# Optimization experiments

Hardware: AMD Instinct MI355X
Metric: run time of the kernel (lower is better)

The kernel has to match this reference:

```python
import jax, jax.numpy as jnp
import numpy as np

B, N, TS, TT, C, H, L = 64, 128, 48, 12, 3, 128, 2


def _u(key, shape, fan):
    s = 1.0 / np.sqrt(fan)
    return jax.random.uniform(key, shape, jnp.float32, -s, s)


def setup_inputs() -> dict:
    key = jax.random.key(0)
    ks = jax.random.split(key, 24)
    return {
        'flow_x': jax.random.normal(ks[0], (B, N, TS, C), jnp.float32),
        'flow_y': jax.random.normal(ks[1], (B, N, TT, C), jnp.float32),
        'enc_w_ih0': _u(ks[2], (3 * H, C), H),
        'enc_w_ih1': _u(ks[3], (3 * H, H), H),
        'enc_w_hh': _u(ks[4], (L, 3 * H, H), H),
        'enc_b_ih': _u(ks[5], (L, 3 * H), H),
        'enc_b_hh': _u(ks[6], (L, 3 * H), H),
        'enc_hid_w': _u(ks[7], (H, H), H),
        'enc_hid_b': _u(ks[8], (H,), H),
        'dec_w_ih0': _u(ks[9], (3 * H, C + H), H),
        'dec_w_ih1': _u(ks[10], (3 * H, H), H),
        'dec_w_hh': _u(ks[11], (L, 3 * H, H), H),
        'dec_b_ih': _u(ks[12], (L, 3 * H), H),
        'dec_b_hh': _u(ks[13], (L, 3 * H), H),
        'attn_w': _u(ks[14], (H, 2 * H), 2 * H),
        'attn_b': _u(ks[15], (H,), 2 * H),
        'v_w': _u(ks[16], (1, H), H),
        'fc_w': _u(ks[17], (C, 2 * H + C), 2 * H + C),
        'fc_b': _u(ks[18], (C,), 2 * H + C),
    }


def gru_cell(x, h, w_ih, w_hh, b_ih, b_hh):
    gi = x @ w_ih.T + b_ih  # [NB, 3H]
    gh = h @ w_hh.T + b_hh
    ir, iz, i_n = jnp.split(gi, 3, axis=-1)
    hr, hz, h_n = jnp.split(gh, 3, axis=-1)
    r = jax.nn.sigmoid(ir + hr)
    z = jax.nn.sigmoid(iz + hz)
    n = jnp.tanh(i_n + r * h_n)
    return (1.0 - z) * n + z * h


def run_gru_layer(xs, h0, w_ih, w_hh, b_ih, b_hh):
    def step(h, x):
        hn = gru_cell(x, h, w_ih, w_hh, b_ih, b_hh)
        return hn, hn
    hT, ys = jax.lax.scan(step, h0, xs)
    return ys, hT


def reference(flow_x, flow_y, enc_w_ih0, enc_w_ih1, enc_w_hh, enc_b_ih, enc_b_hh,
              enc_hid_w, enc_hid_b, dec_w_ih0, dec_w_ih1, dec_w_hh, dec_b_ih,
              dec_b_hh, attn_w, attn_b, v_w, fc_w, fc_b):
    b, n, tt, c = flow_y.shape
    ts = flow_x.shape[2]
    h = enc_hid_w.shape[0]
    nb = n * b
    # fuse (node, batch) -> one batch dim: [TS, N*B, C]
    xs = flow_x.transpose(2, 1, 0, 3).reshape(ts, nb, c)
    h0 = jnp.zeros((nb, h), flow_x.dtype)
    # encoder: 2-layer GRU
    ys0, hT0 = run_gru_layer(xs, h0, enc_w_ih0, enc_w_hh[0], enc_b_ih[0], enc_b_hh[0])
    en_out, hT1 = run_gru_layer(ys0, h0, enc_w_ih1, enc_w_hh[1], enc_b_ih[1], enc_b_hh[1])
    hidden = jnp.tanh(jnp.stack([hT0, hT1]) @ enc_hid_w.T + enc_hid_b)  # [L, NB, H]
    dec_in0 = xs[-1]  # last source step, [NB, C]

    def dec_step(carry, _):
        hid, dec_in = carry
        h_last = hid[1]  # [NB, H]
        # attention over encoder timesteps
        cat = jnp.concatenate(
            [jnp.broadcast_to(h_last, (ts, nb, h)), en_out], axis=-1)  # [TS, NB, 2H]
        energy = jnp.tanh(cat @ attn_w.T + attn_b)
        scores = jnp.squeeze(energy @ v_w.T, -1)  # [TS, NB]
        a = jax.nn.softmax(scores, axis=0)
        context = jnp.einsum('tb,tbh->bh', a, en_out)  # [NB, H]
        x0 = jnp.concatenate([dec_in, context], axis=-1)  # [NB, C+H]
        h0n = gru_cell(x0, hid[0], dec_w_ih0, dec_w_hh[0], dec_b_ih[0], dec_b_hh[0])
        h1n = gru_cell(h0n, hid[1], dec_w_ih1, dec_w_hh[1], dec_b_ih[1], dec_b_hh[1])
        # de_output == hidden[-1] after step, so fc input is [h1n, h1n, dec_in]
        out = jnp.concatenate([h1n, h1n, dec_in], axis=-1) @ fc_w.T + fc_b  # [NB, C]
        return (jnp.stack([h0n, h1n]), out), out

    _, outs = jax.lax.scan(dec_step, (hidden, dec_in0), None, length=tt)
    pred = outs.reshape(tt, n, b, c).transpose(2, 1, 0, 3)  # [B, N, TT, C]
    return pred, flow_y
```

## Files before the change

kernel.cpp:

```cpp
#include <hip/hip_runtime.h>
#include <hip/hip_bf16.h>
#include <math.h>

#define NB   8192
#define TSRC 48
#define TTGT 12
#define ROWS 32
#define DR   16

typedef float f32x4 __attribute__((ext_vector_type(4)));
typedef float f32x2 __attribute__((ext_vector_type(2)));
typedef short bf16x8 __attribute__((ext_vector_type(8)));
typedef short bf16x4 __attribute__((ext_vector_type(4)));

#define QSCALE 2.8853900817779268f

__device__ __forceinline__ float bf2f(unsigned short u){ return __uint_as_float(((unsigned)u)<<16); }
__device__ __forceinline__ unsigned short f2bf(float f){
  unsigned u = __float_as_uint(f);
  u += 0x7fffu + ((u>>16)&1u);
  return (unsigned short)(u>>16);
}
__device__ __forceinline__ float sigm(float x){ return 1.0f/(1.0f+__expf(-x)); }
__device__ __forceinline__ float tanhfast(float x){
  float a = fminf(fabsf(x), 15.0f);
  float e = __expf(2.0f*a);
  float r = 1.0f - 2.0f/(e+1.0f);
  return copysignf(r, x);
}
__device__ __forceinline__ f32x4 mfma16(bf16x8 a, bf16x8 b, f32x4 c){
  return __builtin_amdgcn_mfma_f32_16x16x32_bf16(a,b,c,0,0,0);
}
__device__ __forceinline__ bf16x8 ldsfrag(const short* buf, int lr, int kbase, int koff){
  const int el = (kbase + koff) ^ ((lr&7)<<3);
  return *(const bf16x8*)(buf + lr*128 + el);
}
__device__ __forceinline__ uint2 enc8_fp8(bf16x8 v){
  int t0 = __builtin_amdgcn_cvt_pk_fp8_f32(bf2f((unsigned short)v[0]), bf2f((unsigned short)v[1]), 0, false);
  t0     = __builtin_amdgcn_cvt_pk_fp8_f32(bf2f((unsigned short)v[2]), bf2f((unsigned short)v[3]), t0, true);
  int t1 = __builtin_amdgcn_cvt_pk_fp8_f32(bf2f((unsigned short)v[4]), bf2f((unsigned short)v[5]), 0, false);
  t1     = __builtin_amdgcn_cvt_pk_fp8_f32(bf2f((unsigned short)v[6]), bf2f((unsigned short)v[7]), t1, true);
  uint2 o; o.x = (unsigned)t0; o.y = (unsigned)t1; return o;
}
__device__ __forceinline__ void dec4_fp8(unsigned u, float* out){
  f32x2 lo = __builtin_amdgcn_cvt_pk_f32_fp8((int)u, false);
  f32x2 hi = __builtin_amdgcn_cvt_pk_f32_fp8((int)u, true);
  out[0]=lo.x; out[1]=lo.y; out[2]=hi.x; out[3]=hi.y;
}

__global__ __launch_bounds__(512,2) void enc_mega(
  const float* __restrict__ xs3,
  const unsigned short* __restrict__ Wc0, const unsigned short* __restrict__ Wc1,
  const unsigned short* __restrict__ Wp,
  const float* __restrict__ bih, const float* __restrict__ bhh,
  const float* __restrict__ attn_b,
  unsigned char* __restrict__ en_s, unsigned char* __restrict__ p_s,
  float* __restrict__ hseed0, float* __restrict__ hseed1)
{
  __shared__ float h0f[ROWS][132];
  __shared__ float h1f[ROWS][132];
  __shared__ short h0b[ROWS][128];
  __shared__ short h1b[ROWS][128];
  __shared__ short xfrag[TSRC][ROWS][8];
  __shared__ short ptile[ROWS][128];

  const int bid  = blockIdx.x;
  const int row0 = bid*ROWS;
  const int tid  = threadIdx.x;
  const int lane = tid & 63;
  const int w    = tid >> 6;
  const int l15  = lane & 15;
  const int q4   = lane >> 4;
  const int koff = q4*8;
  const int jcol = w*16 + l15;

  for (int e=tid; e<ROWS*132; e+=512){ int r=e/132, c=e%132; h0f[r][c]=0.f; h1f[r][c]=0.f; }
  for (int e=tid; e<ROWS*128; e+=512){ ((short*)h0b)[e]=0; ((short*)h1b)[e]=0; }
  for (int e=tid; e<TSRC*ROWS; e+=512){
    int t = e/ROWS, r = e%ROWS;
    const float* s = xs3 + ((size_t)t*NB + row0 + r)*3;
    short* d = &xfrag[t][r][0];
    d[0]=(short)f2bf(s[0]); d[1]=(short)f2bf(s[1]); d[2]=(short)f2bf(s[2]);
    d[3]=0; d[4]=0; d[5]=0; d[6]=0; d[7]=0;
  }

  bf16x8 wb0[5][3], wb1[8][3], wp[4];
  #pragma unroll
  for (int g=0; g<3; g++){
    #pragma unroll
    for (int ks=0; ks<5; ks++)
      wb0[ks][g] = *(const bf16x8*)(Wc0 + (size_t)(g*128 + jcol)*160 + ks*32 + koff);
    #pragma unroll
    for (int ks=0; ks<8; ks++)
      wb1[ks][g] = *(const bf16x8*)(Wc1 + (size_t)(g*128 + jcol)*256 + ks*32 + koff);
  }
  #pragma unroll
  for (int ks=0; ks<4; ks++)
    wp[ks] = *(const bf16x8*)(Wp + (size_t)jcol*128 + ks*32 + koff);

  const float bR0 = bih[jcol]     + bhh[jcol];
  const float bZ0 = bih[128+jcol] + bhh[128+jcol];
  const float bNi0= bih[256+jcol];
  const float bNh0= bhh[256+jcol];
  const float bR1 = bih[384+jcol]     + bhh[384+jcol];
  const float bZ1 = bih[384+128+jcol] + bhh[384+128+jcol];
  const float bNi1= bih[384+256+jcol];
  const float bNh1= bhh[384+256+jcol];
  const float pb  = attn_b[jcol];
  const bf16x8 zz = {0,0,0,0,0,0,0,0};
  const f32x4 z4 = {0.f,0.f,0.f,0.f};

  __syncthreads();

  for (int t=0; t<TSRC; t++){
    f32x4 aR[2],aZ[2],aNh[2],aNi[2];
    #pragma unroll
    for (int m=0;m<2;m++){ aR[m]=z4; aZ[m]=z4; aNh[m]=z4; aNi[m]=z4; }
    #pragma unroll
    for (int m=0;m<2;m++){
      const int lr = m*16 + l15;
      #pragma unroll
      for (int ks=0;ks<4;ks++){
        bf16x8 a = ldsfrag(&h0b[0][0], lr, ks*32, koff);
        aR[m]=mfma16(a,wb0[ks][0],aR[m]);
        aZ[m]=mfma16(a,wb0[ks][1],aZ[m]);
        aNh[m]=mfma16(a,wb0[ks][2],aNh[m]);
      }
      bf16x8 ax = zz;
      if (q4==0) ax = *(const bf16x8*)(&xfrag[t][lr][0]);
      aR[m]=mfma16(ax,wb0[4][0],aR[m]);
      aZ[m]=mfma16(ax,wb0[4][1],aZ[m]);
      aNi[m]=mfma16(ax,wb0[4][2],aNi[m]);
    }
    __syncthreads();
    #pragma unroll
    for (int m=0;m<2;m++){
      #pragma unroll
      for (int rr=0;rr<4;rr++){
        int r = m*16 + q4*4 + rr;
        float rg = sigm(aR[m][rr]+bR0);
        float zgg= sigm(aZ[m][rr]+bZ0);
        float ng = tanhfast(aNi[m][rr]+bNi0 + rg*(aNh[m][rr]+bNh0));
        float hn = (1.f-zgg)*ng + zgg*h0f[r][jcol];
        h0f[r][jcol] = hn;
        h0b[r][jcol ^ ((r&7)<<3)] = (short)f2bf(hn);
      }
    }
    __syncthreads();
    #pragma unroll
    for (int m=0;m<2;m++){ aR[m]=z4; aZ[m]=z4; aNh[m]=z4; aNi[m]=z4; }
    #pragma unroll
    for (int m=0;m<2;m++){
      const int lr = m*16 + l15;
      #pragma unroll
      for (int ks=0;ks<4;ks++){
        bf16x8 a = ldsfrag(&h1b[0][0], lr, ks*32, koff);
        aR[m]=mfma16(a,wb1[ks][0],aR[m]);
        aZ[m]=mfma16(a,wb1[ks][1],aZ[m]);
        aNh[m]=mfma16(a,wb1[ks][2],aNh[m]);
      }
      #pragma unroll
      for (int ks=0;ks<4;ks++){
        bf16x8 a = ldsfrag(&h0b[0][0], lr, ks*32, koff);
        aR[m]=mfma16(a,wb1[4+ks][0],aR[m]);
        aZ[m]=mfma16(a,wb1[4+ks][1],aZ[m]);
        aNi[m]=mfma16(a,wb1[4+ks][2],aNi[m]);
      }
    }
    __syncthreads();
    #pragma unroll
    for (int m=0;m<2;m++){
      #pragma unroll
      for (int rr=0;rr<4;rr++){
        int r = m*16 + q4*4 + rr;
        float rg = sigm(aR[m][rr]+bR1);
        float zgg= sigm(aZ[m][rr]+bZ1);
        float ng = tanhfast(aNi[m][rr]+bNi1 + rg*(aNh[m][rr]+bNh1));
        float hn = (1.f-zgg)*ng + zgg*h1f[r][jcol];
        h1f[r][jcol] = hn;
        h1b[r][jcol ^ ((r&7)<<3)] = (short)f2bf(hn);
      }
    }
    __syncthreads();
    f32x4 pacc[2]; pacc[0]=z4; pacc[1]=z4;
    #pragma unroll
    for (int m=0;m<2;m++){
      const int lr = m*16 + l15;
      #pragma unroll
      for (int ks=0;ks<4;ks++){
        bf16x8 a = ldsfrag(&h1b[0][0], lr, ks*32, koff);
        pacc[m]=mfma16(a,wp[ks],pacc[m]);
      }
    }
    #pragma unroll
    for (int m=0;m<2;m++){
      #pragma unroll
      for (int rr=0;rr<4;rr++){
        int r = m*16 + q4*4 + rr;
        ptile[r][jcol] = (short)f2bf((pacc[m][rr] + pb) * QSCALE);
      }
    }
    __syncthreads();
    {
      const int r = tid >> 4, jc = tid & 15, j0 = jc*8;
      bf16x8 ev = *(const bf16x8*)(&h1b[r][j0 ^ ((r&7)<<3)]);
      bf16x8 pv = *(const bf16x8*)(&ptile[r][j0]);
      const size_t base = ((((size_t)bid*TSRC + t)*ROWS + r)<<7) + j0;
      *(uint2*)(en_s + base) = enc8_fp8(ev);
      *(uint2*)(p_s  + base) = enc8_fp8(pv);
    }
  }
  for (int e=tid; e<ROWS*128; e+=512){
    int r = e>>7, c = e&127;
    hseed0[(size_t)(row0+r)*128 + c] = h0f[r][c];
    hseed1[(size_t)(row0+r)*128 + c] = h1f[r][c];
  }
}

__global__ __launch_bounds__(512,4) void dec_mega(
  const float* __restrict__ hseed0, const float* __restrict__ hseed1,
  const unsigned short* __restrict__ Ehw, const float* __restrict__ ehb,
  const float* __restrict__ xs3,
  const unsigned short* __restrict__ Wd0, const unsigned short* __restrict__ Wd1,
  const unsigned short* __restrict__ Wq, const float* __restrict__ v_w,
  const float* __restrict__ bih, const float* __restrict__ bhh,
  const unsigned char* __restrict__ en_s, const unsigned char* __restrict__ p_s,
  const float* __restrict__ fcs, const float* __restrict__ ftail,
  float* __restrict__ pred)
{
  __shared__ short hd0b[DR][128];
  __shared__ short hd1b[DR][128];
  __shared__ float qf[DR][132];
  __shared__ float s_lds[TSRC*DR];
  __shared__ short ctxb[DR][128];
  __shared__ float din[DR][4];
  __shared__ float vls[128];

  const int db   = blockIdx.x;
  const int row0 = db*DR;
  const int tid  = threadIdx.x;
  const int lane = tid & 63;
  const int w    = tid >> 6;
  const int l15  = lane & 15;
  const int q4   = lane >> 4;
  const int koff = q4*8;
  const int jcol = w*16 + l15;
  const f32x4 z4 = {0.f,0.f,0.f,0.f};
  const bf16x8 zz = {0,0,0,0,0,0,0,0};
  const size_t sb0 = (size_t)(db>>1)*TSRC*4096 + (size_t)(db&1)*2048;

  if (tid < 128) vls[tid] = v_w[tid];
  if (tid < DR){
    const float* s = xs3 + ((size_t)(TSRC-1)*NB + row0 + tid)*3;
    din[tid][0]=s[0]; din[tid][1]=s[1]; din[tid][2]=s[2];
  }

  float h0reg[4], h1reg[4];

  {
    const float bb = ehb[jcol];
    #pragma unroll
    for (int L=0; L<2; L++){
      const float* hs = L ? hseed1 : hseed0;
      f32x4 acc = z4;
      #pragma unroll
      for (int ks=0;ks<4;ks++){
        const float* ap = hs + (size_t)(row0+l15)*128 + ks*32 + koff;
        float4 f0 = *(const float4*)(ap);
        float4 f1 = *(const float4*)(ap+4);
        bf16x8 a;
        a[0]=(short)f2bf(f0.x); a[1]=(short)f2bf(f0.y); a[2]=(short)f2bf(f0.z); a[3]=(short)f2bf(f0.w);
        a[4]=(short)f2bf(f1.x); a[5]=(short)f2bf(f1.y); a[6]=(short)f2bf(f1.z); a[7]=(short)f2bf(f1.w);
        bf16x8 b = *(const bf16x8*)(Ehw + (size_t)jcol*128 + ks*32 + koff);
        acc = mfma16(a,b,acc);
      }
      #pragma unroll
      for (int rr=0;rr<4;rr++){
        int r = q4*4 + rr;
        float v = tanhfast(acc[rr] + bb);
        if (L) h1reg[rr] = v; else h0reg[rr] = v;
        short hb = (short)f2bf(v);
        if (L) hd1b[r][jcol ^ ((r&7)<<3)] = hb;
        else   hd0b[r][jcol ^ ((r&7)<<3)] = hb;
      }
    }
  }

  const float bR0 = bih[jcol]     + bhh[jcol];
  const float bZ0 = bih[128+jcol] + bhh[128+jcol];
  const float bNi0= bih[256+jcol];
  const float bNh0= bhh[256+jcol];
  const float bR1 = bih[384+jcol]     + bhh[384+jcol];
  const float bZ1 = bih[384+128+jcol] + bhh[384+128+jcol];
  const float bNi1= bih[384+256+jcol];
  const float bNh1= bhh[384+256+jcol];

  __syncthreads();

  const int jr = l15*8;
  float vreg[8]; float Vpart = 0.f;
  #pragma unroll
  for (int e=0;e<8;e++){ vreg[e] = vls[jr+e]; Vpart += vreg[e]; }

  for (int t=0; t<TTGT; t++){
    {
      f32x4 qa = z4;
      #pragma unroll
      for (int ks=0;ks<4;ks++){
        bf16x8 a = ldsfrag(&hd1b[0][0], l15, ks*32, koff);
        bf16x8 b = *(const bf16x8*)(Wq + (size_t)jcol*128 + ks*32 + koff);
        qa = mfma16(a,b,qa);
      }
      #pragma unroll
      for (int rr=0;rr<4;rr++)
        qf[q4*4+rr][jcol] = qa[rr] * QSCALE;
    }
    __syncthreads();
    {
      int sidx = w*96 + q4;
      const unsigned char* pp = p_s + sb0;
      uint2 pv = *(const uint2*)(pp + (size_t)(sidx>>4)*4096 + (sidx&15)*128 + jr);
      #pragma unroll 4
      for (int k=0;k<24;k++){
        int snext = sidx + 4;
        uint2 pn = pv;
        if (k < 23)
          pn = *(const uint2*)(pp + (size_t)(snext>>4)*4096 + (snext&15)*128 + jr);
        const int r = sidx & 15;
        const float4 q0 = *(const float4*)(&qf[r][jr]);
        const float4 q1 = *(const float4*)(&qf[r][jr+4]);
        float pd[8];
        dec4_fp8(pv.x, pd); dec4_fp8(pv.y, pd+4);
        float s2 = 0.f;
        s2 = fmaf(vreg[0], __builtin_amdgcn_rcpf(__builtin_amdgcn_exp2f(pd[0]+q0.x)+1.f), s2);
        s2 = fmaf(vreg[1], __builtin_amdgcn_rcpf(__builtin_amdgcn_exp2f(pd[1]+q0.y)+1.f), s2);
        s2 = fmaf(vreg[2], __builtin_amdgcn_rcpf(__builtin_amdgcn_exp2f(pd[2]+q0.z)+1.f), s2);
        s2 = fmaf(vreg[3], __builtin_amdgcn_rcpf(__builtin_amdgcn_exp2f(pd[3]+q0.w)+1.f), s2);
        s2 = fmaf(vreg[4], __builtin_amdgcn_rcpf(__builtin_amdgcn_exp2f(pd[4]+q1.x)+1.f), s2);
        s2 = fmaf(vreg[5], __builtin_amdgcn_rcpf(__builtin_amdgcn_exp2f(pd[5]+q1.y)+1.f), s2);
        s2 = fmaf(vreg[6], __builtin_amdgcn_rcpf(__builtin_amdgcn_exp2f(pd[6]+q1.z)+1.f), s2);
        s2 = fmaf(vreg[7], __builtin_amdgcn_rcpf(__builtin_amdgcn_exp2f(pd[7]+q1.w)+1.f), s2);
        float sl = Vpart - 2.f*s2;
        sl += __shfl_xor(sl, 1); sl += __shfl_xor(sl, 2);
        sl += __shfl_xor(sl, 4); sl += __shfl_xor(sl, 8);
        if (l15 == 0) s_lds[sidx] = sl;
        sidx = snext; pv = pn;
      }
    }
    __syncthreads();
    if (tid < DR){
      float sv[TSRC]; float mx = -1e30f;
      #pragma unroll
      for (int k=0;k<TSRC;k++){ sv[k] = s_lds[k*DR+tid]; mx = fmaxf(mx, sv[k]); }
      float den = 0.f;
      #pragma unroll
      for (int k=0;k<TSRC;k++){ float e2 = __expf(sv[k]-mx); sv[k]=e2; den += e2; }
      float rd = 1.0f/den;
      #pragma unroll
      for (int k=0;k<TSRC;k++) s_lds[k*DR+tid] = sv[k]*rd;
    }
    __syncthreads();
    {
      const int cr = 2*w + (lane>>5);
      const int cj = (lane&31)*4;
      const unsigned char* ep = en_s + sb0 + cr*128 + cj;
      float ca0=0.f, ca1=0.f, ca2=0.f, ca3=0.f;
      #pragma unroll 3
      for (int tt=0; tt<TSRC; tt+=4){
        unsigned u0 = *(const unsigned*)(ep + (size_t)(tt  )*4096);
        unsigned u1 = *(const unsigned*)(ep + (size_t)(tt+1)*4096);
        unsigned u2 = *(const unsigned*)(ep + (size_t)(tt+2)*4096);
        unsigned u3 = *(const unsigned*)(ep + (size_t)(tt+3)*4096);
        float a0 = s_lds[(tt  )*DR + cr];
        float a1 = s_lds[(tt+1)*DR + cr];
        float a2 = s_lds[(tt+2)*DR + cr];
        float a3 = s_lds[(tt+3)*DR + cr];
        float d0[4], d1[4], d2[4], d3[4];
        dec4_fp8(u0,d0); dec4_fp8(u1,d1); dec4_fp8(u2,d2); dec4_fp8(u3,d3);
        ca0 += a0*d0[0] + a1*d1[0] + a2*d2[0] + a3*d3[0];
        ca1 += a0*d0[1] + a1*d1[1] + a2*d2[1] + a3*d3[1];
        ca2 += a0*d0[2] + a1*d1[2] + a2*d2[2] + a3*d3[2];
        ca3 += a0*d0[3] + a1*d1[3] + a2*d2[3] + a3*d3[3];
      }
      bf16x4 cv;
      cv[0]=(short)f2bf(ca0); cv[1]=(short)f2bf(ca1);
      cv[2]=(short)f2bf(ca2); cv[3]=(short)f2bf(ca3);
      *(bf16x4*)(&ctxb[cr][cj ^ ((cr&7)<<3)]) = cv;
    }
    __syncthreads();
    {
      f32x4 aR=z4, aZ=z4, aNh=z4, aNi=z4;
      #pragma unroll
      for (int ks=0; ks<9; ks++){
        bf16x8 b0 = *(const bf16x8*)(Wd0 + (size_t)(jcol)*288     + ks*32 + koff);
        bf16x8 b1 = *(const bf16x8*)(Wd0 + (size_t)(128+jcol)*288 + ks*32 + koff);
        bf16x8 b2 = *(const bf16x8*)(Wd0 + (size_t)(256+jcol)*288 + ks*32 + koff);
        bf16x8 a;
        if (ks < 4)       a = ldsfrag(&hd0b[0][0], l15, ks*32, koff);
        else if (ks == 4){
          a = zz;
          if (q4==0){ a[0]=(short)f2bf(din[l15][0]); a[1]=(short)f2bf(din[l15][1]); a[2]=(short)f2bf(din[l15][2]); }
        } else            a = ldsfrag(&ctxb[0][0], l15, (ks-5)*32, koff);
        aR = mfma16(a,b0,aR);
        aZ = mfma16(a,b1,aZ);
        if (ks<4) aNh = mfma16(a,b2,aNh);
        else      aNi = mfma16(a,b2,aNi);
      }
      __syncthreads();
      #pragma unroll
      for (int rr=0;rr<4;rr++){
        int r = q4*4 + rr;
        float rg = sigm(aR[rr]+bR0);
        float zg = sigm(aZ[rr]+bZ0);
        float ng = tanhfast(aNi[rr]+bNi0 + rg*(aNh[rr]+bNh0));
        float hn = (1.f-zg)*ng + zg*h0reg[rr];
        h0reg[rr] = hn;
        hd0b[r][jcol ^ ((r&7)<<3)] = (short)f2bf(hn);
      }
    }
    __syncthreads();
    {
      f32x4 aR=z4, aZ=z4, aNh=z4, aNi=z4;
      #pragma unroll
      for (int ks=0; ks<8; ks++){
        bf16x8 b0 = *(const bf16x8*)(Wd1 + (size_t)(jcol)*256     + ks*32 + koff);
        bf16x8 b1 = *(const bf16x8*)(Wd1 + (size_t)(128+jcol)*256 + ks*32 + koff);
        bf16x8 b2 = *(const bf16x8*)(Wd1 + (size_t)(256+jcol)*256 + ks*32 + koff);
        bf16x8 a = (ks<4) ? ldsfrag(&hd1b[0][0], l15, ks*32, koff)
                          : ldsfrag(&hd0b[0][0], l15, (ks-4)*32, koff);
        aR = mfma16(a,b0,aR);
        aZ = mfma16(a,b1,aZ);
        if (ks<4) aNh = mfma16(a,b2,aNh);
        else      aNi = mfma16(a,b2,aNi);
      }
      __syncthreads();
      #pragma unroll
      for (int rr=0;rr<4;rr++){
        int r = q4*4 + rr;
        float rg = sigm(aR[rr]+bR1);
        float zg = sigm(aZ[rr]+bZ1);
        float ng = tanhfast(aNi[rr]+bNi1 + rg*(aNh[rr]+bNh1));
        float hn = (1.f-zg)*ng + zg*h1reg[rr];
        h1reg[rr] = hn;
        hd1b[r][jcol ^ ((r&7)<<3)] = (short)f2bf(hn);
      }
    }
    __syncthreads();
    if (tid < 16*DR){
      const int fr = tid >> 4, fu = tid & 15, fj0 = fu*8;
      bf16x8 hv8 = *(const bf16x8*)(&hd1b[fr][fj0 ^ ((fr&7)<<3)]);
      float hv[8];
      #pragma unroll
      for (int e=0;e<8;e++) hv[e] = bf2f((unsigned short)hv8[e]);
      float o0=0.f,o1=0.f,o2=0.f;
      {
        float4 wa = *(const float4*)(fcs + fj0);
        float4 wb = *(const float4*)(fcs + fj0 + 4);
        o0 = wa.x*hv[0]+wa.y*hv[1]+wa.z*hv[2]+wa.w*hv[3]
           + wb.x*hv[4]+wb.y*hv[5]+wb.z*hv[6]+wb.w*hv[7];
      }
      {
        float4 wa = *(const float4*)(fcs + 132 + fj0);
        float4 wb = *(const float4*)(fcs + 132 + fj0 + 4);
        o1 = wa.x*hv[0]+wa.y*hv[1]+wa.z*hv[2]+wa.w*hv[3]
           + wb.x*hv[4]+wb.y*hv[5]+wb.z*hv[6]+wb.w*hv[7];
      }
      {
        float4 wa = *(const float4*)(fcs + 264 + fj0);
        float4 wb = *(const float4*)(fcs + 264 + fj0 + 4);
        o2 = wa.x*hv[0]+wa.y*hv[1]+wa.z*hv[2]+wa.w*hv[3]
           + wb.x*hv[4]+wb.y*hv[5]+wb.z*hv[6]+wb.w*hv[7];
      }
      #pragma unroll
      for (int off=1; off<16; off<<=1){
        o0 += __shfl_xor(o0, off);
        o1 += __shfl_xor(o1, off);
        o2 += __shfl_xor(o2, off);
      }
      if (fu == 0){
        float d0 = din[fr][0], d1 = din[fr][1], d2 = din[fr][2];
        o0 += ftail[3]  + ftail[0]*d0 + ftail[1]*d1 + ftail[2]*d2;
        o1 += ftail[7]  + ftail[4]*d0 + ftail[5]*d1 + ftail[6]*d2;
        o2 += ftail[11] + ftail[8]*d0 + ftail[9]*d1 + ftail[10]*d2;
        const int nb = row0 + fr;
        const int n = nb >> 6, b = nb & 63;
        float* pr = pred + ((size_t)(b*128 + n)*TTGT + t)*3;
        pr[0]=o0; pr[1]=o1; pr[2]=o2;
        din[fr][0]=o0; din[fr][1]=o1; din[fr][2]=o2;
      }
    }
    __syncthreads();
  }
}

__global__ __launch_bounds__(256) void build_kernel(
  const float* __restrict__ e_ih0, const float* __restrict__ e_ih1,
  const float* __restrict__ e_hh,
  const float* __restrict__ d_ih0, const float* __restrict__ d_ih1,
  const float* __restrict__ d_hh,
  const float* __restrict__ attn_w, const float* __restrict__ ehw_f,
  const float* __restrict__ fc_w, const float* __restrict__ fc_b,
  unsigned short* __restrict__ Wc_e0, unsigned short* __restrict__ Wc_e1,
  unsigned short* __restrict__ Wc_d0, unsigned short* __restrict__ Wc_d1,
  unsigned short* __restrict__ Wq, unsigned short* __restrict__ Wp,
  unsigned short* __restrict__ Ehw,
  float* __restrict__ fcs, float* __restrict__ ftail)
{
  int idx = blockIdx.x*256 + threadIdx.x;
  if (idx >= 418200) return;
  if (idx < 61440){
    int j = idx/160, k = idx%160;
    float v = (k<128) ? e_hh[(size_t)j*128 + k]
            : (k<131) ? e_ih0[j*3 + (k-128)] : 0.0f;
    Wc_e0[idx] = f2bf(v);
  } else if (idx < 159744){
    int i = idx - 61440; int j = i/256, k = i%256;
    float v = (k<128) ? e_hh[(size_t)(384 + j)*128 + k]
                      : e_ih1[(size_t)j*128 + (k-128)];
    Wc_e1[i] = f2bf(v);
  } else if (idx < 270336){
    int i = idx - 159744; int j = i/288, k = i%288;
    float v = (k<128) ? d_hh[(size_t)j*128 + k]
            : (k<131) ? d_ih0[(size_t)j*131 + (k-128)]
            : (k<160) ? 0.0f
                      : d_ih0[(size_t)j*131 + 3 + (k-160)];
    Wc_d0[i] = f2bf(v);
  } else if (idx < 368640){
    int i = idx - 270336; int j = i/256, k = i%256;
    float v = (k<128) ? d_hh[(size_t)(384 + j)*128 + k]
                      : d_ih1[(size_t)j*128 + (k-128)];
    Wc_d1[i] = f2bf(v);
  } else if (idx < 385024){
    int i = idx - 368640; int j = i/128, k = i%128;
    Wq[i] = f2bf(attn_w[(size_t)j*256 + k]);
  } else if (idx < 401408){
    int i = idx - 385024; int j = i/128, k = i%128;
    Wp[i] = f2bf(attn_w[(size_t)j*256 + 128 + k]);
  } else if (idx < 417792){
    int i = idx - 401408;
    Ehw[i] = f2bf(ehw_f[i]);
  } else if (idx < 418188){
    int i = idx - 417792; int g = i/132, j = i%132;
    fcs[i] = (j<128) ? (fc_w[(size_t)g*259 + j] + fc_w[(size_t)g*259 + 128 + j]) : 0.0f;
  } else {
    int i = idx - 418188; int g = i/4, e = i%4;
    ftail[i] = (e<3) ? fc_w[(size_t)g*259 + 256 + e] : fc_b[g];
  }
}

__global__ __launch_bounds__(256) void pack_kernel(
  const float* __restrict__ fx, float* __restrict__ xs3)
{
  int idx = blockIdx.x*256 + threadIdx.x;
  if (idx >= TSRC*NB) return;
  int nb = idx & (NB-1), t = idx >> 13;
  int n = nb >> 6, b = nb & 63;
  const float* s = fx + (((size_t)(b*128) + n)*TSRC + t)*3;
  float* d = xs3 + (size_t)idx*3;
  d[0]=s[0]; d[1]=s[1]; d[2]=s[2];
}

extern "C" void kernel_launch(void* const* d_in, const int* in_sizes, int n_in,
                              void* d_out, int out_size, void* d_ws, size_t ws_size,
                              hipStream_t stream)
{
  const float* flow_x   = (const float*)d_in[0];
  const float* flow_y   = (const float*)d_in[1];
  const float* enc_w_ih0= (const float*)d_in[2];
  const float* enc_w_ih1= (const float*)d_in[3];
  const float* enc_w_hh = (const float*)d_in[4];
  const float* enc_b_ih = (const float*)d_in[5];
  const float* enc_b_hh = (const float*)d_in[6];
  const float* enc_hid_w= (const float*)d_in[7];
  const float* enc_hid_b= (const float*)d_in[8];
  const float* dec_w_ih0= (const float*)d_in[9];
  const float* dec_w_ih1= (const float*)d_in[10];
  const float* dec_w_hh = (const float*)d_in[11];
  const float* dec_b_ih = (const float*)d_in[12];
  const float* dec_b_hh = (const float*)d_in[13];
  const float* attn_w   = (const float*)d_in[14];
  const float* attn_b   = (const float*)d_in[15];
  const float* v_w      = (const float*)d_in[16];
  const float* fc_w     = (const float*)d_in[17];
  const float* fc_b     = (const float*)d_in[18];

  float* out_pred = (float*)d_out;
  float* out_fy   = out_pred + (size_t)64*128*TTGT*3;

  char* ws = (char*)d_ws;
  size_t off = 0;
  auto alloc = [&](size_t bytes)->void* {
    void* pp = ws + off; off += (bytes + 255) & ~(size_t)255; return pp;
  };
  float*          xs3    = (float*)alloc((size_t)TSRC*NB*3*4);
  unsigned char*  en_s   = (unsigned char*)alloc((size_t)TSRC*NB*128);
  unsigned char*  p_s    = (unsigned char*)alloc((size_t)TSRC*NB*128);
  float*          hseed0 = (float*)alloc((size_t)NB*128*4);
  float*          hseed1 = (float*)alloc((size_t)NB*128*4);
  unsigned short* Wc_e0  = (unsigned short*)alloc((size_t)384*160*2);
  unsigned short* Wc_e1  = (unsigned short*)alloc((size_t)384*256*2);
  unsigned short* Wc_d0  = (unsigned short*)alloc((size_t)384*288*2);
  unsigned short* Wc_d1  = (unsigned short*)alloc((size_t)384*256*2);
  unsigned short* attnWq = (unsigned short*)alloc((size_t)128*128*2);
  unsigned short* attnWp = (unsigned short*)alloc((size_t)128*128*2);
  unsigned short* Ehw    = (unsigned short*)alloc((size_t)128*128*2);
  float*          fcs    = (float*)alloc((size_t)3*132*4);
  float*          ftail  = (float*)alloc((size_t)12*4);

  hipMemcpyAsync(out_fy, flow_y, (size_t)64*128*TTGT*3*4,
                 hipMemcpyDeviceToDevice, stream);
  build_kernel<<<1634, 256, 0, stream>>>(
      enc_w_ih0, enc_w_ih1, enc_w_hh, dec_w_ih0, dec_w_ih1, dec_w_hh,
      attn_w, enc_hid_w, fc_w, fc_b,
      Wc_e0, Wc_e1, Wc_d0, Wc_d1, attnWq, attnWp, Ehw, fcs, ftail);
  pack_kernel<<<1536, 256, 0, stream>>>(flow_x, xs3);

  enc_mega<<<NB/ROWS, 512, 0, stream>>>(
      xs3, Wc_e0, Wc_e1, attnWp, enc_b_ih, enc_b_hh, attn_b,
      en_s, p_s, hseed0, hseed1);

  dec_mega<<<NB/DR, 512, 0, stream>>>(
      hseed0, hseed1, Ehw, enc_hid_b, xs3, Wc_d0, Wc_d1, attnWq, v_w,
      dec_b_ih, dec_b_hh, en_s, p_s, fcs, ftail, out_pred);
}
```

Before: 1.188 ms.

## Shrink decoder tile to 8 rows, stage encoder fp8 tensors and weights on-chip

The decoder now processes 8 rows per block instead of 16, so twice as many blocks run. Each block first copies its fp8 attention-projection and encoder-output slices into shared memory and reads them from there in the score and context loops. Layer-1 GRU weights and the query weights are held in registers for all timesteps instead of being reloaded from global memory each step. Softmax is now a wave-parallel shuffle reduction, and launch bounds drop to one block per CU. The cost is wasted MFMA rows (16-row tiles with only 8 valid), heavier register and LDS use that lowers occupancy, and more blocks doing duplicated weight loads.

```diff
diff --git a/kernel.cpp b/kernel.cpp
--- a/kernel.cpp
+++ b/kernel.cpp
@@ -6,7 +6,7 @@
 #define TSRC 48
 #define TTGT 12
 #define ROWS 32
-#define DR   16
+#define DR   8
 
 typedef float f32x4 __attribute__((ext_vector_type(4)));
 typedef float f32x2 __attribute__((ext_vector_type(2)));
@@ -217,7 +217,7 @@
   }
 }
 
-__global__ __launch_bounds__(512,4) void dec_mega(
+__global__ __launch_bounds__(512,1) void dec_mega(
   const float* __restrict__ hseed0, const float* __restrict__ hseed1,
   const unsigned short* __restrict__ Ehw, const float* __restrict__ ehb,
   const float* __restrict__ xs3,
@@ -228,6 +228,8 @@
   const float* __restrict__ fcs, const float* __restrict__ ftail,
   float* __restrict__ pred)
 {
+  __shared__ unsigned char p8[TSRC*DR*128];
+  __shared__ unsigned char e8[TSRC*DR*128];
   __shared__ short hd0b[DR][128];
   __shared__ short hd1b[DR][128];
   __shared__ float qf[DR][132];
@@ -242,13 +244,25 @@
   const int lane = tid & 63;
   const int w    = tid >> 6;
   const int l15  = lane & 15;
+  const int lr8  = l15 & 7;
   const int q4   = lane >> 4;
   const int koff = q4*8;
   const int jcol = w*16 + l15;
   const f32x4 z4 = {0.f,0.f,0.f,0.f};
   const bf16x8 zz = {0,0,0,0,0,0,0,0};
-  const size_t sb0 = (size_t)(db>>1)*TSRC*4096 + (size_t)(db&1)*2048;
-
+
+  {
+    const size_t gb = (size_t)(db>>2)*TSRC*4096 + (size_t)(db&3)*1024;
+    const unsigned char* gp = p_s + gb;
+    const unsigned char* ge = en_s + gb;
+    #pragma unroll
+    for (int i=0;i<6;i++){
+      int c = tid + i*512;
+      int t = c >> 6, cc = c & 63;
+      *(uint4*)(p8 + c*16) = *(const uint4*)(gp + (size_t)t*4096 + cc*16);
+      *(uint4*)(e8 + c*16) = *(const uint4*)(ge + (size_t)t*4096 + cc*16);
+    }
+  }
   if (tid < 128) vls[tid] = v_w[tid];
   if (tid < DR){
     const float* s = xs3 + ((size_t)(TSRC-1)*NB + row0 + tid)*3;
@@ -265,7 +279,7 @@
       f32x4 acc = z4;
       #pragma unroll
       for (int ks=0;ks<4;ks++){
-        const float* ap = hs + (size_t)(row0+l15)*128 + ks*32 + koff;
+        const float* ap = hs + (size_t)(row0+lr8)*128 + ks*32 + koff;
         float4 f0 = *(const float4*)(ap);
         float4 f1 = *(const float4*)(ap+4);
         bf16x8 a;
@@ -274,17 +288,29 @@
         bf16x8 b = *(const bf16x8*)(Ehw + (size_t)jcol*128 + ks*32 + koff);
         acc = mfma16(a,b,acc);
       }
-      #pragma unroll
-      for (int rr=0;rr<4;rr++){
-        int r = q4*4 + rr;
-        float v = tanhfast(acc[rr] + bb);
-        if (L) h1reg[rr] = v; else h0reg[rr] = v;
-        short hb = (short)f2bf(v);
-        if (L) hd1b[r][jcol ^ ((r&7)<<3)] = hb;
-        else   hd0b[r][jcol ^ ((r&7)<<3)] = hb;
-      }
-    }
-  }
+      if (q4 < 2){
+        #pragma unroll
+        for (int rr=0;rr<4;rr++){
+          int r = q4*4 + rr;
+          float v = tanhfast(acc[rr] + bb);
+          if (L) h1reg[rr] = v; else h0reg[rr] = v;
+          short hb = (short)f2bf(v);
+          if (L) hd1b[r][jcol ^ ((r&7)<<3)] = hb;
+          else   hd0b[r][jcol ^ ((r&7)<<3)] = hb;
+        }
+      }
+    }
+  }
+
+  bf16x8 wd1[8][3], wq[4];
+  #pragma unroll
+  for (int g=0; g<3; g++)
+    #pragma unroll
+    for (int ks=0; ks<8; ks++)
+      wd1[ks][g] = *(const bf16x8*)(Wd1 + (size_t)(g*128 + jcol)*256 + ks*32 + koff);
+  #pragma unroll
+  for (int ks=0; ks<4; ks++)
+    wq[ks] = *(const bf16x8*)(Wq + (size_t)jcol*128 + ks*32 + koff);
 
   const float bR0 = bih[jcol]     + bhh[jcol];
   const float bZ0 = bih[128+jcol] + bhh[128+jcol];
@@ -307,26 +333,22 @@
       f32x4 qa = z4;
       #pragma unroll
       for (int ks=0;ks<4;ks++){
-        bf16x8 a = ldsfrag(&hd1b[0][0], l15, ks*32, koff);
-        bf16x8 b = *(const bf16x8*)(Wq + (size_t)jcol*128 + ks*32 + koff);
-        qa = mfma16(a,b,qa);
-      }
-      #pragma unroll
-      for (int rr=0;rr<4;rr++)
-        qf[q4*4+rr][jcol] = qa[rr] * QSCALE;
+        bf16x8 a = ldsfrag(&hd1b[0][0], lr8, ks*32, koff);
+        qa = mfma16(a,wq[ks],qa);
+      }
+      if (q4 < 2){
+        #pragma unroll
+        for (int rr=0;rr<4;rr++)
+          qf[q4*4+rr][jcol] = qa[rr] * QSCALE;
+      }
     }
     __syncthreads();
     {
-      int sidx = w*96 + q4;
-      const unsigned char* pp = p_s + sb0;
-      uint2 pv = *(const uint2*)(pp + (size_t)(sidx>>4)*4096 + (sidx&15)*128 + jr);
-      #pragma unroll 4
-      for (int k=0;k<24;k++){
-        int snext = sidx + 4;
-        uint2 pn = pv;
-        if (k < 23)
-          pn = *(const uint2*)(pp + (size_t)(snext>>4)*4096 + (snext&15)*128 + jr);
-        const int r = sidx & 15;
+      #pragma unroll
+      for (int i=0;i<12;i++){
+        const int sidx = w*48 + i*4 + q4;
+        const int r = sidx & 7;
+        uint2 pv = *(const uint2*)(p8 + sidx*128 + jr);
         const float4 q0 = *(const float4*)(&qf[r][jr]);
         const float4 q1 = *(const float4*)(&qf[r][jr+4]);
         float pd[8];
@@ -344,48 +366,43 @@
         sl += __shfl_xor(sl, 1); sl += __shfl_xor(sl, 2);
         sl += __shfl_xor(sl, 4); sl += __shfl_xor(sl, 8);
         if (l15 == 0) s_lds[sidx] = sl;
-        sidx = snext; pv = pn;
-      }
-    }
-    __syncthreads();
-    if (tid < DR){
-      float sv[TSRC]; float mx = -1e30f;
-      #pragma unroll
-      for (int k=0;k<TSRC;k++){ sv[k] = s_lds[k*DR+tid]; mx = fmaxf(mx, sv[k]); }
-      float den = 0.f;
-      #pragma unroll
-      for (int k=0;k<TSRC;k++){ float e2 = __expf(sv[k]-mx); sv[k]=e2; den += e2; }
-      float rd = 1.0f/den;
-      #pragma unroll
-      for (int k=0;k<TSRC;k++) s_lds[k*DR+tid] = sv[k]*rd;
+      }
     }
     __syncthreads();
     {
-      const int cr = 2*w + (lane>>5);
-      const int cj = (lane&31)*4;
-      const unsigned char* ep = en_s + sb0 + cr*128 + cj;
+      float s = (lane < TSRC) ? s_lds[lane*DR + w] : -1e30f;
+      float mx = s;
+      #pragma unroll
+      for (int off=32; off>=1; off>>=1) mx = fmaxf(mx, __shfl_xor(mx, off));
+      float e2 = (lane < TSRC) ? __expf(s - mx) : 0.f;
+      float den = e2;
+      #pragma unroll
+      for (int off=32; off>=1; off>>=1) den += __shfl_xor(den, off);
+      if (lane < TSRC) s_lds[lane*DR + w] = e2 / den;
+    }
+    __syncthreads();
+    {
+      const int lh = lane >> 5;
+      const int cj = (lane & 31) * 4;
+      const unsigned char* ep = e8 + w*128 + cj;
       float ca0=0.f, ca1=0.f, ca2=0.f, ca3=0.f;
-      #pragma unroll 3
-      for (int tt=0; tt<TSRC; tt+=4){
-        unsigned u0 = *(const unsigned*)(ep + (size_t)(tt  )*4096);
-        unsigned u1 = *(const unsigned*)(ep + (size_t)(tt+1)*4096);
-        unsigned u2 = *(const unsigned*)(ep + (size_t)(tt+2)*4096);
-        unsigned u3 = *(const unsigned*)(ep + (size_t)(tt+3)*4096);
-        float a0 = s_lds[(tt  )*DR + cr];
-        float a1 = s_lds[(tt+1)*DR + cr];
-        float a2 = s_lds[(tt+2)*DR + cr];
-        float a3 = s_lds[(tt+3)*DR + cr];
-        float d0[4], d1[4], d2[4], d3[4];
-        dec4_fp8(u0,d0); dec4_fp8(u1,d1); dec4_fp8(u2,d2); dec4_fp8(u3,d3);
-        ca0 += a0*d0[0] + a1*d1[0] + a2*d2[0] + a3*d3[0];
-        ca1 += a0*d0[1] + a1*d1[1] + a2*d2[1] + a3*d3[1];
-        ca2 += a0*d0[2] + a1*d1[2] + a2*d2[2] + a3*d3[2];
-        ca3 += a0*d0[3] + a1*d1[3] + a2*d2[3] + a3*d3[3];
-      }
-      bf16x4 cv;
-      cv[0]=(short)f2bf(ca0); cv[1]=(short)f2bf(ca1);
-      cv[2]=(short)f2bf(ca2); cv[3]=(short)f2bf(ca3);
-      *(bf16x4*)(&ctxb[cr][cj ^ ((cr&7)<<3)]) = cv;
+      #pragma unroll
+      for (int k=0; k<24; k++){
+        const int tt = 2*k + lh;
+        unsigned u = *(const unsigned*)(ep + tt*1024);
+        float a = s_lds[tt*DR + w];
+        float d[4];
+        dec4_fp8(u, d);
+        ca0 += a*d[0]; ca1 += a*d[1]; ca2 += a*d[2]; ca3 += a*d[3];
+      }
+      ca0 += __shfl_xor(ca0, 32); ca1 += __shfl_xor(ca1, 32);
+      ca2 += __shfl_xor(ca2, 32); ca3 += __shfl_xor(ca3, 32);
+      if (lh == 0){
+        bf16x4 cv;
+        cv[0]=(short)f2bf(ca0); cv[1]=(short)f2bf(ca1);
+        cv[2]=(short)f2bf(ca2); cv[3]=(short)f2bf(ca3);
+        *(bf16x4*)(&ctxb[w][cj ^ ((w&7)<<3)]) = cv;
+      }
     }
     __syncthreads();
     {
@@ -396,53 +413,59 @@
         bf16x8 b1 = *(const bf16x8*)(Wd0 + (size_t)(128+jcol)*288 + ks*32 + koff);
         bf16x8 b2 = *(const bf16x8*)(Wd0 + (size_t)(256+jcol)*288 + ks*32 + koff);
         bf16x8 a;
-        if (ks < 4)       a = ldsfrag(&hd0b[0][0], l15, ks*32, koff);
+        if (ks < 4)       a = ldsfrag(&hd0b[0][0], lr8, ks*32, koff);
         else if (ks == 4){
           a = zz;
-          if (q4==0){ a[0]=(short)f2bf(din[l15][0]); a[1]=(short)f2bf(din[l15][1]); a[2]=(short)f2bf(din[l15][2]); }
-        } else            a = ldsfrag(&ctxb[0][0], l15, (ks-5)*32, koff);
+          if (q4==0){ a[0]=(short)f2bf(din[lr8][0]); a[1]=(short)f2bf(din[lr8][1]); a[2]=(short)f2bf(din[lr8][2]); }
+        } else            a = ldsfrag(&ctxb[0][0], lr8, (ks-5)*32, koff);
         aR = mfma16(a,b0,aR);
         aZ = mfma16(a,b1,aZ);
         if (ks<4) aNh = mfma16(a,b2,aNh);
         else      aNi = mfma16(a,b2,aNi);
       }
       __syncthreads();
-      #pragma unroll
-      for (int rr=0;rr<4;rr++){
-        int r = q4*4 + rr;
-        float rg = sigm(aR[rr]+bR0);
-        float zg = sigm(aZ[rr]+bZ0);
-        float ng = tanhfast(aNi[rr]+bNi0 + rg*(aNh[rr]+bNh0));
-        float hn = (1.f-zg)*ng + zg*h0reg[rr];
-        h0reg[rr] = hn;
-        hd0b[r][jcol ^ ((r&7)<<3)] = (short)f2bf(hn);
+      if (q4 < 2){
+        #pragma unroll
+        for (int rr=0;rr<4;rr++){
+          int r = q4*4 + rr;
+          float rg = sigm(aR[rr]+bR0);
+          float zg = sigm(aZ[rr]+bZ0);
+          float ng = tanhfast(aNi[rr]+bNi0 + rg*(aNh[rr]+bNh0));
+          float hn = (1.f-zg)*ng + zg*h0reg[rr];
+          h0reg[rr] = hn;
+          hd0b[r][jcol ^ ((r&7)<<3)] = (short)f2bf(hn);
+        }
       }
     }
     __syncthreads();
     {
       f32x4 aR=z4, aZ=z4, aNh=z4, aNi=z4;
       #pragma unroll
-      for (int ks=0; ks<8; ks++){
-        bf16x8 b0 = *(const bf16x8*)(Wd1 + (size_t)(jcol)*256     + ks*32 + koff);
-        bf16x8 b1 = *(const bf16x8*)(Wd1 + (size_t)(128+jcol)*256 + ks*32 + koff);
-        bf16x8 b2 = *(const bf16x8*)(Wd1 + (size_t)(256+jcol)*256 + ks*32 + koff);
-        bf16x8 a = (ks<4) ? ldsfrag(&hd1b[0][0], l15, ks*32, koff)
-                          : ldsfrag(&hd0b[0][0], l15, (ks-4)*32, koff);
-        aR = mfma16(a,b0,aR);
-        aZ = mfma16(a,b1,aZ);
-        if (ks<4) aNh = mfma16(a,b2,aNh);
-        else      aNi = mfma16(a,b2,aNi);
+      for (int ks=0; ks<4; ks++){
+        bf16x8 a = ldsfrag(&hd1b[0][0], lr8, ks*32, koff);
+        aR = mfma16(a,wd1[ks][0],aR);
+        aZ = mfma16(a,wd1[ks][1],aZ);
+        aNh= mfma16(a,wd1[ks][2],aNh);
+      }
+      #pragma unroll
+      for (int ks=0; ks<4; ks++){
+        bf16x8 a = ldsfrag(&hd0b[0][0], lr8, ks*32, koff);
+        aR = mfma16(a,wd1[4+ks][0],aR);
+        aZ = mfma16(a,wd1[4+ks][1],aZ);
+        aNi= mfma16(a,wd1[4+ks][2],aNi);
       }
       __syncthreads();
-      #pragma unroll
-      for (int rr=0;rr<4;rr++){
-        int r = q4*4 + rr;
-        float rg = sigm(aR[rr]+bR1);
-        float zg = sigm(aZ[rr]+bZ1);
-        float ng = tanhfast(aNi[rr]+bNi1 + rg*(aNh[rr]+bNh1));
-        float hn = (1.f-zg)*ng + zg*h1reg[rr];
-        h1reg[rr] = hn;
-        hd1b[r][jcol ^ ((r&7)<<3)] = (short)f2bf(hn);
+      if (q4 < 2){
+        #pragma unroll
+        for (int rr=0;rr<4;rr++){
+          int r = q4*4 + rr;
+          float rg = sigm(aR[rr]+bR1);
+          float zg = sigm(aZ[rr]+bZ1);
+          float ng = tanhfast(aNi[rr]+bNi1 + rg*(aNh[rr]+bNh1));
+          float hn = (1.f-zg)*ng + zg*h1reg[rr];
+          h1reg[rr] = hn;
+          hd1b[r][jcol ^ ((r&7)<<3)] = (short)f2bf(hn);
+        }
       }
     }
     __syncthreads();
```

After: 1.553 ms. +30.7%, slower.
